# Kernel optimization log

Hardware: AMD Instinct MI355X
Metric: run time of the kernel (lower is better)

Reference implementation:

```python
import math
import jax, jax.numpy as jnp
import numpy as np

B, N, D = 256, 64, 64
H, HEAD = D // 4, 4
UNTANH = 0.6
SHARPNESS = 1.0
BSCALE = math.sqrt(2 + math.sqrt(2))
INPUT_DIM = 100
SINK_ITERS = 10
EPS = 1e-8


def buntanh(x, a, s):
    # blended (bounded + un-)tanh: tanh(x) + a*x, variance-rescaled
    return (jnp.tanh(x) + a * x) / s


def rms_norm(x, axes):
    return x * jax.lax.rsqrt(jnp.mean(x * x, axis=axes, keepdims=True) + 1e-6)


def sinkhorn_knopp(x, iters=SINK_ITERS):
    # stable exp then alternating row/col normalization -> ~doubly stochastic
    p = jnp.exp(x - jnp.max(x, axis=(-1, -2), keepdims=True))
    def body(p, _):
        p = p / (jnp.sum(p, axis=-1, keepdims=True) + EPS)
        p = p / (jnp.sum(p, axis=-2, keepdims=True) + EPS)
        return p, None
    p, _ = jax.lax.scan(body, p, None, length=iters)
    return p


def setup_inputs() -> dict:
    key = jax.random.key(0)
    k1, k2, k3, k4, k5 = jax.random.split(key, 5)
    env_input = jax.random.normal(k1, (B, INPUT_DIM), dtype=jnp.float32)
    state = 1e-5 * jax.random.normal(k2, (B, N, D), dtype=jnp.float32)
    scale = 1.0 / math.sqrt(D)
    w1 = jax.random.normal(k3, (B, N, D, D), dtype=jnp.float32) * scale
    w2 = jax.random.normal(k4, (B, N, D, D), dtype=jnp.float32) * scale
    w3 = jax.random.normal(k5, (B, N, D, D), dtype=jnp.float32) * scale
    return {"env_input": env_input, "state": state, "w1": w1, "w2": w2, "w3": w3}


def reference(env_input, state, w1, w2, w3):
    step_state = state  # buffer clone
    prediction = buntanh(jnp.einsum('bnj,bnjk->bnk', step_state, w1), UNTANH, BSCALE)
    keys = buntanh(jnp.einsum('bnj,bnjk->bnk', step_state, w2), UNTANH, BSCALE)
    queries = buntanh(jnp.einsum('bnj,bnjk->bnk', step_state, w3), UNTANH, BSCALE)

    # torch.no_grad() block -> stop_gradient over the whole routing/target calc
    Q = queries.reshape(B, N, H, HEAD).transpose(0, 2, 1, 3)  # [B,H,N,hd]
    K = keys.reshape(B, N, H, HEAD).transpose(0, 2, 1, 3)
    V = prediction.reshape(B, N, H, HEAD).transpose(0, 2, 1, 3)
    raw_A = jnp.einsum('bhnd,bhmd->bhnm', Q, K) / math.sqrt(HEAD)
    raw_A = rms_norm(raw_A, axes=(-1, -2)) * SHARPNESS
    probs = sinkhorn_knopp(raw_A)
    A = jnp.where(probs > 1.0 / N, probs, 0.0)  # sinkhot forward (k-hot)
    routed_V = jnp.einsum('bhnm,bhmd->bhnd', A, V)
    target = routed_V.transpose(0, 2, 1, 3).reshape(B, N, D)

    num_input_nodes = math.ceil(INPUT_DIM / D)
    pad_len = num_input_nodes * D - INPUT_DIM
    env_pad = jnp.pad(env_input, ((0, 0), (0, pad_len))).reshape(B, num_input_nodes, D)
    target = target.at[:, :num_input_nodes, :].set(env_pad)
    target = jax.lax.stop_gradient(target)

    loss_w1 = jnp.mean((prediction - target) ** 2)
    loss_w2 = jnp.mean((keys - step_state) ** 2)
    loss_w3 = jnp.mean((queries - target) ** 2)
    return loss_w1 + loss_w2 + loss_w3
```

## Files before the change

### kernel.cpp

```cpp
#include <hip/hip_runtime.h>
#include <math.h>

#define TOT (256*64*64)
#define EPS_SINK 1e-8f
#define THR (1.0f/64.0f)
#define INV_BSCALE 0.5412658773652741f
#define UNTANH_A 0.6f

typedef float nativef4 __attribute__((ext_vector_type(4)));

static __device__ __forceinline__ float buntanh(float x) {
    return (tanhf(x) + UNTANH_A * x) * INV_BSCALE;
}

#if __has_builtin(__builtin_amdgcn_rcpf)
static __device__ __forceinline__ float fastrcp(float x) {
    return __builtin_amdgcn_rcpf(x);
}
#else
static __device__ __forceinline__ float fastrcp(float x) { return 1.0f / x; }
#endif

__global__ __launch_bounds__(1024, 4)
__attribute__((amdgpu_waves_per_eu(4, 4)))
void fused_brain_kernel(
    const float* __restrict__ env, const float* __restrict__ state,
    const float* __restrict__ w1, const float* __restrict__ w2,
    const float* __restrict__ w3, float* __restrict__ part)
{
    __shared__ float Vh[64][65];
    __shared__ float Kh[64][65];
    __shared__ float Qh[64][65];
    __shared__ float redL[16][3];

    const int b    = blockIdx.x;
    const int wave = threadIdx.x >> 6;
    const int l    = threadIdx.x & 63;
    const int k4   = l & 15;
    const int jg   = l >> 4;

#pragma unroll 2
    for (int tt = 0; tt < 12; ++tt) {
        const int task = wave * 12 + tt;
        const int widx = task >> 6;
        const int n    = task & 63;
        const float* __restrict__ w =
            (widx == 0) ? w1 : (widx == 1) ? w2 : w3;
        const size_t bn = (size_t)(b * 64 + n);

        const float* sp = state + bn * 64 + jg * 16;
        float s[16];
#pragma unroll
        for (int i = 0; i < 4; ++i) {
            const float4 v = *(const float4*)(sp + 4 * i);
            s[4 * i + 0] = v.x; s[4 * i + 1] = v.y;
            s[4 * i + 2] = v.z; s[4 * i + 3] = v.w;
        }

        const nativef4* wp = (const nativef4*)(w + bn * 4096 +
                                               (size_t)(jg * 16) * 64 + k4 * 4);
        float a0 = 0.f, a1 = 0.f, a2 = 0.f, a3 = 0.f;
#pragma unroll
        for (int jj = 0; jj < 16; ++jj) {
            const nativef4 wv = __builtin_nontemporal_load(wp + jj * 16);
            a0 = fmaf(s[jj], wv.x, a0);
            a1 = fmaf(s[jj], wv.y, a1);
            a2 = fmaf(s[jj], wv.z, a2);
            a3 = fmaf(s[jj], wv.w, a3);
        }
        a0 += __shfl_xor(a0, 16, 64); a0 += __shfl_xor(a0, 32, 64);
        a1 += __shfl_xor(a1, 16, 64); a1 += __shfl_xor(a1, 32, 64);
        a2 += __shfl_xor(a2, 16, 64); a2 += __shfl_xor(a2, 32, 64);
        a3 += __shfl_xor(a3, 16, 64); a3 += __shfl_xor(a3, 32, 64);
        if (jg == 0) {
            float* dst = (widx == 0) ? &Vh[n][4 * k4]
                       : (widx == 1) ? &Kh[n][4 * k4] : &Qh[n][4 * k4];
            dst[0] = buntanh(a0);
            dst[1] = buntanh(a1);
            dst[2] = buntanh(a2);
            dst[3] = buntanh(a3);
        }
    }
    __syncthreads();

    const int cb = 4 * wave;
    const int rg = l >> 3;
    const int cg = l & 7;

    float p[8][8];
    float ss = 0.f, mx = -1e30f;
    {
        float kq[8][4];
#pragma unroll
        for (int j = 0; j < 8; ++j)
#pragma unroll
            for (int d = 0; d < 4; ++d)
                kq[j][d] = Kh[8 * cg + j][cb + d];
#pragma unroll
        for (int i = 0; i < 8; ++i) {
            const float q0 = Qh[8 * rg + i][cb + 0];
            const float q1 = Qh[8 * rg + i][cb + 1];
            const float q2 = Qh[8 * rg + i][cb + 2];
            const float q3 = Qh[8 * rg + i][cb + 3];
#pragma unroll
            for (int j = 0; j < 8; ++j) {
                const float e = (q0 * kq[j][0] + q1 * kq[j][1] +
                                 q2 * kq[j][2] + q3 * kq[j][3]) * 0.5f;
                p[i][j] = e;
                ss += e * e;
                mx = fmaxf(mx, e);
            }
        }
    }
#pragma unroll
    for (int o = 1; o <= 32; o <<= 1) {
        ss += __shfl_xor(ss, o, 64);
        mx = fmaxf(mx, __shfl_xor(mx, o, 64));
    }
    const float scale = rsqrtf(ss * (1.0f / 4096.0f) + 1e-6f);

#pragma unroll
    for (int i = 0; i < 8; ++i)
#pragma unroll
        for (int j = 0; j < 8; ++j)
            p[i][j] = __expf(scale * (p[i][j] - mx));

    for (int it = 0; it < 10; ++it) {
#pragma unroll
        for (int i = 0; i < 8; ++i) {
            float r = ((p[i][0] + p[i][1]) + (p[i][2] + p[i][3])) +
                      ((p[i][4] + p[i][5]) + (p[i][6] + p[i][7]));
            r += __shfl_xor(r, 1, 64);
            r += __shfl_xor(r, 2, 64);
            r += __shfl_xor(r, 4, 64);
            const float inv = fastrcp(r + EPS_SINK);
#pragma unroll
            for (int j = 0; j < 8; ++j) p[i][j] *= inv;
        }
#pragma unroll
        for (int j = 0; j < 8; ++j) {
            float c = ((p[0][j] + p[1][j]) + (p[2][j] + p[3][j])) +
                      ((p[4][j] + p[5][j]) + (p[6][j] + p[7][j]));
            c += __shfl_xor(c, 8, 64);
            c += __shfl_xor(c, 16, 64);
            c += __shfl_xor(c, 32, 64);
            const float inv = fastrcp(c + EPS_SINK);
#pragma unroll
            for (int i = 0; i < 8; ++i) p[i][j] *= inv;
        }
    }

#pragma unroll
    for (int i = 0; i < 8; ++i)
#pragma unroll
        for (int j = 0; j < 8; ++j)
            p[i][j] = (p[i][j] > THR) ? p[i][j] : 0.f;

    float tva0 = 0.f, tva1 = 0.f, tva2 = 0.f, tva3 = 0.f;
#pragma unroll
    for (int grp = 0; grp < 2; ++grp) {
        float og[4][4];
#pragma unroll
        for (int i = 0; i < 4; ++i)
#pragma unroll
            for (int d = 0; d < 4; ++d) og[i][d] = 0.f;

#pragma unroll
        for (int jh = 0; jh < 8; jh += 4) {
            float vf[4][4];
#pragma unroll
            for (int j = 0; j < 4; ++j)
#pragma unroll
                for (int d = 0; d < 4; ++d)
                    vf[j][d] = Vh[8 * cg + jh + j][cb + d];
#pragma unroll
            for (int i = 0; i < 4; ++i)
#pragma unroll
                for (int j = 0; j < 4; ++j) {
                    og[i][0] = fmaf(p[4 * grp + i][jh + j], vf[j][0], og[i][0]);
                    og[i][1] = fmaf(p[4 * grp + i][jh + j], vf[j][1], og[i][1]);
                    og[i][2] = fmaf(p[4 * grp + i][jh + j], vf[j][2], og[i][2]);
                    og[i][3] = fmaf(p[4 * grp + i][jh + j], vf[j][3], og[i][3]);
                }
        }
#pragma unroll
        for (int i = 0; i < 4; ++i)
#pragma unroll
            for (int d = 0; d < 4; ++d) {
                float v = og[i][d];
                v += __shfl_xor(v, 1, 64);
                v += __shfl_xor(v, 2, 64);
                v += __shfl_xor(v, 4, 64);
                og[i][d] = v;
            }
        if ((cg >> 2) == grp) {
#pragma unroll
            for (int i = 0; i < 4; ++i) {
                if ((cg & 3) == i) {
                    tva0 = og[i][0]; tva1 = og[i][1];
                    tva2 = og[i][2]; tva3 = og[i][3];
                }
            }
        }
    }

    float l1 = 0.f, l2 = 0.f, l3 = 0.f;
    {
        const int n = 8 * rg + cg;
        const float* srow = state + ((size_t)(b * 64 + n)) * 64;
#pragma unroll
        for (int d = 0; d < 4; ++d) {
            const int c = cb + d;
            float tv;
            if (n < 2) {
                const int idx = n * 64 + c;
                tv = (idx < 100) ? env[b * 100 + idx] : 0.f;
            } else {
                tv = (d == 0) ? tva0 : (d == 1) ? tva1 : (d == 2) ? tva2 : tva3;
            }
            const float pv = Vh[n][c];
            const float kk = Kh[n][c];
            const float qv = Qh[n][c];
            const float sv = srow[c];
            const float d1 = pv - tv;
            const float d2 = kk - sv;
            const float d3 = qv - tv;
            l1 = fmaf(d1, d1, l1);
            l2 = fmaf(d2, d2, l2);
            l3 = fmaf(d3, d3, l3);
        }
    }
#pragma unroll
    for (int o = 1; o <= 32; o <<= 1) {
        l1 += __shfl_xor(l1, o, 64);
        l2 += __shfl_xor(l2, o, 64);
        l3 += __shfl_xor(l3, o, 64);
    }
    if (l == 0) { redL[wave][0] = l1; redL[wave][1] = l2; redL[wave][2] = l3; }
    __syncthreads();
    if (threadIdx.x == 0) {
        float s1 = 0.f, s2 = 0.f, s3 = 0.f;
#pragma unroll
        for (int wv = 0; wv < 16; ++wv) {
            s1 += redL[wv][0]; s2 += redL[wv][1]; s3 += redL[wv][2];
        }
        part[b]       = s1;
        part[256 + b] = s2;
        part[512 + b] = s3;
    }
}

__global__ __launch_bounds__(256) void loss_final_kernel(
    const float* __restrict__ part, float* __restrict__ out)
{
    float a = 0.f;
    for (int i = threadIdx.x; i < 768; i += 256) a += part[i];
#pragma unroll
    for (int o = 32; o >= 1; o >>= 1) a += __shfl_xor(a, o, 64);
    __shared__ float red[4];
    const int wv = threadIdx.x >> 6, ln = threadIdx.x & 63;
    if (ln == 0) red[wv] = a;
    __syncthreads();
    if (threadIdx.x == 0) {
        out[0] = (red[0] + red[1] + red[2] + red[3]) * (1.0f / (float)TOT);
    }
}

extern "C" void kernel_launch(void* const* d_in, const int* in_sizes, int n_in,
                              void* d_out, int out_size, void* d_ws, size_t ws_size,
                              hipStream_t stream)
{
    const float* env   = (const float*)d_in[0];
    const float* state = (const float*)d_in[1];
    const float* w1    = (const float*)d_in[2];
    const float* w2    = (const float*)d_in[3];
    const float* w3    = (const float*)d_in[4];
    float* out = (float*)d_out;
    float* part = (float*)d_ws;

    hipLaunchKernelGGL(fused_brain_kernel, dim3(256), dim3(1024), 0, stream,
                       env, state, w1, w2, w3, part);
    hipLaunchKernelGGL(loss_final_kernel, dim3(1), dim3(256), 0, stream,
                       part, out);
}
```

Before: 169.3 us.

## Overlap W1 value GEMV with Sinkhorn routing by splitting waves into roles

The K and Q projections are now computed first by all 16 waves. Afterwards, waves 12-15 compute the V (w1) projection while waves 0-11 run their heads' attention-score and Sinkhorn work; waves 12-15 then do their own heads after a barrier. The aim is to hide the memory-bound w1 streaming behind the compute-bound Sinkhorn loop. The waves_per_eu attribute is also dropped. The risk is load imbalance: four waves stream a third of the weights and then still run Sinkhorn serially, which may lengthen the critical path.

```diff
diff --git a/kernel.cpp b/kernel.cpp
--- a/kernel.cpp
+++ b/kernel.cpp
@@ -21,9 +21,7 @@
 static __device__ __forceinline__ float fastrcp(float x) { return 1.0f / x; }
 #endif
 
-__global__ __launch_bounds__(1024, 4)
-__attribute__((amdgpu_waves_per_eu(4, 4)))
-void fused_brain_kernel(
+__global__ __launch_bounds__(1024, 4) void fused_brain_kernel(
     const float* __restrict__ env, const float* __restrict__ state,
     const float* __restrict__ w1, const float* __restrict__ w2,
     const float* __restrict__ w3, float* __restrict__ part)
@@ -38,16 +36,12 @@
     const int l    = threadIdx.x & 63;
     const int k4   = l & 15;
     const int jg   = l >> 4;
-
-#pragma unroll 2
-    for (int tt = 0; tt < 12; ++tt) {
-        const int task = wave * 12 + tt;
-        const int widx = task >> 6;
-        const int n    = task & 63;
-        const float* __restrict__ w =
-            (widx == 0) ? w1 : (widx == 1) ? w2 : w3;
+    const int rg   = l >> 3;
+    const int cg   = l & 7;
+
+    auto gemv_task = [&](const float* __restrict__ w, float (*dst)[65],
+                         const int n) {
         const size_t bn = (size_t)(b * 64 + n);
-
         const float* sp = state + bn * 64 + jg * 16;
         float s[16];
 #pragma unroll
@@ -56,7 +50,6 @@
             s[4 * i + 0] = v.x; s[4 * i + 1] = v.y;
             s[4 * i + 2] = v.z; s[4 * i + 3] = v.w;
         }
-
         const nativef4* wp = (const nativef4*)(w + bn * 4096 +
                                                (size_t)(jg * 16) * 64 + k4 * 4);
         float a0 = 0.f, a1 = 0.f, a2 = 0.f, a3 = 0.f;
@@ -73,89 +66,108 @@
         a2 += __shfl_xor(a2, 16, 64); a2 += __shfl_xor(a2, 32, 64);
         a3 += __shfl_xor(a3, 16, 64); a3 += __shfl_xor(a3, 32, 64);
         if (jg == 0) {
-            float* dst = (widx == 0) ? &Vh[n][4 * k4]
-                       : (widx == 1) ? &Kh[n][4 * k4] : &Qh[n][4 * k4];
-            dst[0] = buntanh(a0);
-            dst[1] = buntanh(a1);
-            dst[2] = buntanh(a2);
-            dst[3] = buntanh(a3);
-        }
-    }
-    __syncthreads();
+            dst[n][4 * k4 + 0] = buntanh(a0);
+            dst[n][4 * k4 + 1] = buntanh(a1);
+            dst[n][4 * k4 + 2] = buntanh(a2);
+            dst[n][4 * k4 + 3] = buntanh(a3);
+        }
+    };
+
+    float p[8][8];
+
+    auto attn_part1 = [&](const int h) {
+        const int cb = 4 * h;
+        float ss = 0.f, mx = -1e30f;
+        {
+            float kq[8][4];
+#pragma unroll
+            for (int j = 0; j < 8; ++j)
+#pragma unroll
+                for (int d = 0; d < 4; ++d)
+                    kq[j][d] = Kh[8 * cg + j][cb + d];
+#pragma unroll
+            for (int i = 0; i < 8; ++i) {
+                const float q0 = Qh[8 * rg + i][cb + 0];
+                const float q1 = Qh[8 * rg + i][cb + 1];
+                const float q2 = Qh[8 * rg + i][cb + 2];
+                const float q3 = Qh[8 * rg + i][cb + 3];
+#pragma unroll
+                for (int j = 0; j < 8; ++j) {
+                    const float e = (q0 * kq[j][0] + q1 * kq[j][1] +
+                                     q2 * kq[j][2] + q3 * kq[j][3]) * 0.5f;
+                    p[i][j] = e;
+                    ss += e * e;
+                    mx = fmaxf(mx, e);
+                }
+            }
+        }
+#pragma unroll
+        for (int o = 1; o <= 32; o <<= 1) {
+            ss += __shfl_xor(ss, o, 64);
+            mx = fmaxf(mx, __shfl_xor(mx, o, 64));
+        }
+        const float scale = rsqrtf(ss * (1.0f / 4096.0f) + 1e-6f);
+
+#pragma unroll
+        for (int i = 0; i < 8; ++i)
+#pragma unroll
+            for (int j = 0; j < 8; ++j)
+                p[i][j] = __expf(scale * (p[i][j] - mx));
+
+        for (int it = 0; it < 10; ++it) {
+#pragma unroll
+            for (int i = 0; i < 8; ++i) {
+                float r = ((p[i][0] + p[i][1]) + (p[i][2] + p[i][3])) +
+                          ((p[i][4] + p[i][5]) + (p[i][6] + p[i][7]));
+                r += __shfl_xor(r, 1, 64);
+                r += __shfl_xor(r, 2, 64);
+                r += __shfl_xor(r, 4, 64);
+                const float inv = fastrcp(r + EPS_SINK);
+#pragma unroll
+                for (int j = 0; j < 8; ++j) p[i][j] *= inv;
+            }
+#pragma unroll
+            for (int j = 0; j < 8; ++j) {
+                float c = ((p[0][j] + p[1][j]) + (p[2][j] + p[3][j])) +
+                          ((p[4][j] + p[5][j]) + (p[6][j] + p[7][j]));
+                c += __shfl_xor(c, 8, 64);
+                c += __shfl_xor(c, 16, 64);
+                c += __shfl_xor(c, 32, 64);
+                const float inv = fastrcp(c + EPS_SINK);
+#pragma unroll
+                for (int i = 0; i < 8; ++i) p[i][j] *= inv;
+            }
+        }
+
+#pragma unroll
+        for (int i = 0; i < 8; ++i)
+#pragma unroll
+            for (int j = 0; j < 8; ++j)
+                p[i][j] = (p[i][j] > THR) ? p[i][j] : 0.f;
+    };
+
+#pragma unroll 2
+    for (int tt = 0; tt < 8; ++tt) {
+        const int task = 64 + wave * 8 + tt;
+        const int widx = task >> 6;
+        const int n    = task & 63;
+        gemv_task(widx == 1 ? w2 : w3, widx == 1 ? Kh : Qh, n);
+    }
+    __syncthreads();
+
+    if (wave >= 12) {
+#pragma unroll 2
+        for (int tt = 0; tt < 16; ++tt) {
+            gemv_task(w1, Vh, (wave - 12) * 16 + tt);
+        }
+    } else {
+        attn_part1(wave);
+    }
+    __syncthreads();
+
+    if (wave >= 12) attn_part1(wave);
 
     const int cb = 4 * wave;
-    const int rg = l >> 3;
-    const int cg = l & 7;
-
-    float p[8][8];
-    float ss = 0.f, mx = -1e30f;
-    {
-        float kq[8][4];
-#pragma unroll
-        for (int j = 0; j < 8; ++j)
-#pragma unroll
-            for (int d = 0; d < 4; ++d)
-                kq[j][d] = Kh[8 * cg + j][cb + d];
-#pragma unroll
-        for (int i = 0; i < 8; ++i) {
-            const float q0 = Qh[8 * rg + i][cb + 0];
-            const float q1 = Qh[8 * rg + i][cb + 1];
-            const float q2 = Qh[8 * rg + i][cb + 2];
-            const float q3 = Qh[8 * rg + i][cb + 3];
-#pragma unroll
-            for (int j = 0; j < 8; ++j) {
-                const float e = (q0 * kq[j][0] + q1 * kq[j][1] +
-                                 q2 * kq[j][2] + q3 * kq[j][3]) * 0.5f;
-                p[i][j] = e;
-                ss += e * e;
-                mx = fmaxf(mx, e);
-            }
-        }
-    }
-#pragma unroll
-    for (int o = 1; o <= 32; o <<= 1) {
-        ss += __shfl_xor(ss, o, 64);
-        mx = fmaxf(mx, __shfl_xor(mx, o, 64));
-    }
-    const float scale = rsqrtf(ss * (1.0f / 4096.0f) + 1e-6f);
-
-#pragma unroll
-    for (int i = 0; i < 8; ++i)
-#pragma unroll
-        for (int j = 0; j < 8; ++j)
-            p[i][j] = __expf(scale * (p[i][j] - mx));
-
-    for (int it = 0; it < 10; ++it) {
-#pragma unroll
-        for (int i = 0; i < 8; ++i) {
-            float r = ((p[i][0] + p[i][1]) + (p[i][2] + p[i][3])) +
-                      ((p[i][4] + p[i][5]) + (p[i][6] + p[i][7]));
-            r += __shfl_xor(r, 1, 64);
-            r += __shfl_xor(r, 2, 64);
-            r += __shfl_xor(r, 4, 64);
-            const float inv = fastrcp(r + EPS_SINK);
-#pragma unroll
-            for (int j = 0; j < 8; ++j) p[i][j] *= inv;
-        }
-#pragma unroll
-        for (int j = 0; j < 8; ++j) {
-            float c = ((p[0][j] + p[1][j]) + (p[2][j] + p[3][j])) +
-                      ((p[4][j] + p[5][j]) + (p[6][j] + p[7][j]));
-            c += __shfl_xor(c, 8, 64);
-            c += __shfl_xor(c, 16, 64);
-            c += __shfl_xor(c, 32, 64);
-            const float inv = fastrcp(c + EPS_SINK);
-#pragma unroll
-            for (int i = 0; i < 8; ++i) p[i][j] *= inv;
-        }
-    }
-
-#pragma unroll
-    for (int i = 0; i < 8; ++i)
-#pragma unroll
-        for (int j = 0; j < 8; ++j)
-            p[i][j] = (p[i][j] > THR) ? p[i][j] : 0.f;
-
     float tva0 = 0.f, tva1 = 0.f, tva2 = 0.f, tva3 = 0.f;
 #pragma unroll
     for (int grp = 0; grp < 2; ++grp) {
```

Result: faster. 152.8 us (median of 2 runs) (-9.7%).
